# Performance work log

Hardware: AMD Instinct MI355X
Metric: run time of the kernel (lower is better)

The kernel has to match this reference:

```python
import jax, jax.numpy as jnp
import numpy as np

B, S, HID, NH, D = 8, 1024, 768, 12, 64
LENGTHS = np.array([1024, 896, 768, 640, 1024, 512, 768, 896], dtype=np.int64)


def setup_inputs() -> dict:
    key = jax.random.key(0)
    k1, k2 = jax.random.split(key)
    total = int(LENGTHS.sum())  # 6528

    cu_seqlens = jnp.asarray(np.concatenate([[0], np.cumsum(LENGTHS)]), dtype=jnp.int32)
    # flattened (b*s) positions of valid tokens, per flash-attn bert_padding
    indices = jnp.asarray(
        np.concatenate([b * S + np.arange(L) for b, L in enumerate(LENGTHS)]),
        dtype=jnp.int64)
    # 0 = valid token, 1 = pad (original checks attn_mask == 0 for valid)
    attn_mask = jnp.asarray(
        (np.arange(S)[None, :] >= LENGTHS[:, None]).astype(np.int32))

    hidden_states = jax.random.normal(k1, (total, HID), dtype=jnp.float32) * 0.02
    Wqkv_w = jax.random.normal(k2, (3 * HID, HID), dtype=jnp.float32) * 0.02
    Wqkv_b = jnp.zeros((3 * HID,), dtype=jnp.float32)

    # ALiBi bias fused with padding mask, as mosaic passes alibi_attn_mask
    slopes = 2.0 ** (-8.0 * np.arange(1, NH + 1) / NH)  # (NH,)
    pos = np.arange(S)
    rel = -np.abs(pos[None, :] - pos[:, None]).astype(np.float32)  # (S,S)
    alibi_hss = slopes[:, None, None].astype(np.float32) * rel      # (NH,S,S)
    pad_bias = np.where(np.asarray(attn_mask)[:, None, None, :] == 0, 0.0, -10000.0)
    alibi = jnp.asarray(alibi_hss[None] + pad_bias, dtype=jnp.float32)  # (B,NH,S,S)

    return {
        "hidden_states": hidden_states,
        "Wqkv_w": Wqkv_w,
        "Wqkv_b": Wqkv_b,
        "alibi": alibi,
        "cu_seqlens": cu_seqlens,
        "max_seqlen_in_batch": S,
        "indices": indices,
        "attn_mask": attn_mask,
    }


def reference(hidden_states, Wqkv_w, Wqkv_b, alibi, cu_seqlens,
              max_seqlen_in_batch, indices, attn_mask):
    batch = cu_seqlens.shape[0] - 1
    s = max_seqlen_in_batch
    nh = alibi.shape[1]
    d = hidden_states.shape[1] // nh

    # packed QKV projection on unpadded tokens: (nnz, 3*hid)
    qkv = hidden_states @ Wqkv_w.T + Wqkv_b
    # pad_input: scatter into (b*s, 3*hid), then view (b, s, 3, h, d)
    qkv_pad = jnp.zeros((batch * s, qkv.shape[-1]), dtype=qkv.dtype).at[indices].set(qkv)
    qkv_pad = qkv_pad.reshape(batch, s, 3, nh, d)
    q, k, v = qkv_pad[:, :, 0], qkv_pad[:, :, 1], qkv_pad[:, :, 2]  # (b, s, h, d)

    scale = 1.0 / jnp.sqrt(jnp.asarray(d, dtype=q.dtype))
    scores = jnp.einsum('bshd,bthd->bhst', q, k) * scale + alibi  # (b, h, s, s)
    probs = jax.nn.softmax(scores, axis=-1)
    ctx = jnp.einsum('bhst,bthd->bshd', probs, v)  # (b, s, h, d)

    # unpad_input: gather valid tokens back to (nnz, h*d)
    ctx = ctx.reshape(batch * s, nh * d)[indices]
    return ctx
```

## Files before the change

kernel.cpp:

```cpp
#include <hip/hip_runtime.h>
#include <hip/hip_bf16.h>
#include <stdint.h>


typedef __attribute__((ext_vector_type(8))) __bf16 bf16x8;
typedef __attribute__((ext_vector_type(8))) short short8;
typedef __attribute__((ext_vector_type(4))) short short4v;
typedef __attribute__((ext_vector_type(4))) float f32x4;
typedef __attribute__((ext_vector_type(2))) unsigned int u32x2;
typedef unsigned int u32;

#define AS1 __attribute__((address_space(1)))
#define AS3 __attribute__((address_space(3)))

static __device__ __forceinline__ unsigned short f2bf(float x) {
  unsigned u = __builtin_bit_cast(unsigned, x);
  u += 0x7fffu + ((u >> 16) & 1u);
  return (unsigned short)(u >> 16);
}
static __device__ __forceinline__ bf16x8 ld8s(const short* p) {
  return __builtin_bit_cast(bf16x8, *(const short8*)p);
}
static __device__ __forceinline__ u32 cvtpk(float lo, float hi) {
  u32 r;
  asm("v_cvt_pk_bf16_f32 %0, %1, %2" : "=v"(r) : "v"(lo), "v"(hi));
  return r;
}
static __device__ __forceinline__ f32x4 mfma16(u32x2 a, u32x2 b, f32x4 c) {
  asm("v_mfma_f32_16x16x16_bf16 %0, %1, %2, %0" : "+v"(c) : "v"(a), "v"(b));
  return c;
}
static __device__ __forceinline__ float vexp2(float x) {
  float r;
  asm("v_exp_f32 %0, %1" : "=v"(r) : "v"(x));
  return r;
}

__device__ const float g_slope[12] = {
  0.6299605249f, 0.3968502630f, 0.25f,          0.1574901312f,
  0.0992125657f, 0.0625f,       0.0393725328f,  0.0248031414f,
  0.015625f,     0.0098431332f, 0.0062007854f,  0.00390625f
};

__global__ __launch_bounds__(256) void convert_in(
    const float* __restrict__ hidden, const float* __restrict__ W,
    short* __restrict__ hb, short* __restrict__ wb)
{
  constexpr int NA = 6528 * 768;
  constexpr int NW = 2304 * 768;
  const int tot4 = (NA + NW) / 4;
  for (int idx = blockIdx.x * 256 + threadIdx.x; idx < tot4; idx += gridDim.x * 256) {
    const int e0 = idx * 4;
    const float* src; short* dst; int off;
    if (e0 < NA) { src = hidden; dst = hb; off = e0; }
    else         { src = W;      dst = wb; off = e0 - NA; }
    f32x4 v = *((const f32x4*)(src + off));
    short4v o;
    o[0] = (short)f2bf(v[0]); o[1] = (short)f2bf(v[1]);
    o[2] = (short)f2bf(v[2]); o[3] = (short)f2bf(v[3]);
    *(short4v*)(dst + off) = o;
  }
}

__global__ __launch_bounds__(256, 2) void qkv_gemm(
    const short* __restrict__ A, const short* __restrict__ W,
    const float* __restrict__ bias,
    short* __restrict__ qws, short* __restrict__ kws, short* __restrict__ vtws)
{
  constexpr int CUb[9] = {0,1024,1920,2688,3328,4352,4864,5632,6528};
  __shared__ __align__(16) short As[256 * 64];
  __shared__ __align__(16) short Bs[128 * 64];
  const int tid  = threadIdx.x;
  const int lane = tid & 63, w = tid >> 6;
  const int g = lane >> 4, c = lane & 15;
  const int wm = w >> 1, wn = w & 1;
  const int bm = blockIdx.x, bn = blockIdx.y;

  const short* Ab = A + (size_t)bm * 256 * 768;
  const short* Wb = W + (size_t)bn * 128 * 768;

  f32x4 acc[8][4] = {};
  const int sR8 = lane >> 3;
  const int sC8 = (lane & 7) ^ sR8;

  for (int kt = 0; kt < 12; ++kt) {
    if (kt) __syncthreads();
#pragma unroll
    for (int i = 0; i < 8; ++i) {
      const int j = w * 8 + i;
      const AS1 unsigned int* ga =
        (const AS1 unsigned int*)(Ab + (size_t)(j * 8 + sR8) * 768 + kt * 64 + sC8 * 8);
      __builtin_amdgcn_global_load_lds(ga, (AS3 unsigned int*)&As[j * 512], 16, 0, 0);
    }
#pragma unroll
    for (int i = 0; i < 4; ++i) {
      const int j = w * 4 + i;
      const AS1 unsigned int* gb =
        (const AS1 unsigned int*)(Wb + (size_t)(j * 8 + sR8) * 768 + kt * 64 + sC8 * 8);
      __builtin_amdgcn_global_load_lds(gb, (AS3 unsigned int*)&Bs[j * 512], 16, 0, 0);
    }
    __syncthreads();

#pragma unroll
    for (int kh = 0; kh < 2; ++kh) {
      const int xg = (((kh * 4 + g) ^ (c & 7)) << 3);
      bf16x8 bfr[4];
#pragma unroll
      for (int nt = 0; nt < 4; ++nt)
        bfr[nt] = ld8s(&Bs[(wn * 64 + nt * 16 + c) * 64 + xg]);
#pragma unroll
      for (int mt = 0; mt < 8; ++mt) {
        bf16x8 af = ld8s(&As[(wm * 128 + mt * 16 + c) * 64 + xg]);
#pragma unroll
        for (int nt = 0; nt < 4; ++nt)
          acc[mt][nt] = __builtin_amdgcn_mfma_f32_16x16x32_bf16(af, bfr[nt], acc[mt][nt], 0, 0, 0);
      }
    }
  }

  const int row0 = bm * 256 + wm * 128;
  if (row0 >= 6528) return;
  int b = 0;
#pragma unroll
  for (int i = 0; i < 8; ++i) if (row0 >= CUb[i + 1]) b = i + 1;
  const int col0  = bn * 128 + wn * 64;
  const int which = col0 / 768;
  const int hh    = (col0 % 768) / 64;
  const int srow0 = row0 - CUb[b];

  float bb[4];
#pragma unroll
  for (int nt = 0; nt < 4; ++nt) bb[nt] = bias[col0 + nt * 16 + c];

  if (which < 2) {
    const float sc = which ? 1.0f : 0.18033688011112042f;
    short* dst = (which ? kws : qws) + (size_t)(b * 12 + hh) * 1024 * 64;
#pragma unroll
    for (int mt = 0; mt < 8; ++mt)
#pragma unroll
      for (int nt = 0; nt < 4; ++nt)
#pragma unroll
        for (int r = 0; r < 4; ++r) {
          const int s = srow0 + mt * 16 + g * 4 + r;
          dst[(size_t)s * 64 + nt * 16 + c] = (short)f2bf((acc[mt][nt][r] + bb[nt]) * sc);
        }
  } else {
    short* dst = vtws + (size_t)(b * 12 + hh) * 64 * 1024;
#pragma unroll
    for (int mt = 0; mt < 8; ++mt)
#pragma unroll
      for (int nt = 0; nt < 4; ++nt) {
        const int s = srow0 + mt * 16 + g * 4;
        short4v pk;
        pk[0] = (short)f2bf(acc[mt][nt][0] + bb[nt]);
        pk[1] = (short)f2bf(acc[mt][nt][1] + bb[nt]);
        pk[2] = (short)f2bf(acc[mt][nt][2] + bb[nt]);
        pk[3] = (short)f2bf(acc[mt][nt][3] + bb[nt]);
        *(short4v*)&dst[(size_t)(nt * 16 + c) * 1024 + s] = pk;
      }
  }
}

__global__ __launch_bounds__(256, 2) void attn(
    const short* __restrict__ qws, const short* __restrict__ kws,
    const short* __restrict__ vtws, float* __restrict__ out)
{
  constexpr int CU[9]  = {0,1024,1920,2688,3328,4352,4864,5632,6528};
  constexpr int CQT[9] = {0,8,15,21,26,34,38,44,51};
  __shared__ __align__(16) short Ks[2][64 * 64];
  __shared__ __align__(16) short Vs[2][64 * 64];
  const int tid = threadIdx.x, lane = tid & 63, w = tid >> 6;
  const int g = lane >> 4, c = lane & 15;
  const int h = blockIdx.y;
  const int gq = blockIdx.x;
  int b = 0;
#pragma unroll
  for (int i = 0; i < 8; ++i) if (gq >= CQT[i + 1]) b = i + 1;
  const int qt = gq - CQT[b];
  const int Lb = CU[b + 1] - CU[b];
  const int sb = qt * 128 + w * 32;
  const size_t bh = (size_t)(b * 12 + h) * 1024 * 64;
  const short* qp = qws + bh;
  const short* kp = kws + bh;
  const short* vp = vtws + bh;
  const float slope2 = g_slope[h] * 1.4426950408889634f;

  const int sRow = lane >> 3;
  const int sChk = (lane & 7) ^ (sRow & 7);

  bf16x8 qf[2][2];
#pragma unroll
  for (int qh = 0; qh < 2; ++qh)
#pragma unroll
    for (int ks = 0; ks < 2; ++ks)
      qf[qh][ks] = ld8s(qp + (size_t)(sb + qh * 16 + c) * 64 + ks * 32 + g * 8);

  float srowf[2];
#pragma unroll
  for (int qh = 0; qh < 2; ++qh) srowf[qh] = (float)(sb + qh * 16 + c);

  f32x4 accO[2][4] = {};
  float l_part[2] = {};

  auto kaddr = [&](int row, int chunk) { return row * 64 + ((chunk ^ (row & 7)) << 3); };
  auto vaddr = [&](int row, int nt) {
    return row * 64 + (((2 * nt + (g >> 1)) ^ (row & 7)) << 3) + ((g & 1) << 2);
  };

#pragma unroll
  for (int i = 0; i < 2; ++i) {
    const int j = w * 2 + i;
    const int row = j * 8 + sRow;
    const AS1 unsigned int* gk =
      (const AS1 unsigned int*)(kp + (size_t)row * 64 + sChk * 8);
    __builtin_amdgcn_global_load_lds(gk, (AS3 unsigned int*)&Ks[0][j * 512], 16, 0, 0);
    const AS1 unsigned int* gv =
      (const AS1 unsigned int*)(vp + (size_t)row * 1024 + sChk * 8);
    __builtin_amdgcn_global_load_lds(gv, (AS3 unsigned int*)&Vs[0][j * 512], 16, 0, 0);
  }
  __syncthreads();

  int cur = 0;
  for (int t0 = 0; t0 < Lb; t0 += 64) {
    if (t0 + 64 < Lb) {
#pragma unroll
      for (int i = 0; i < 2; ++i) {
        const int j = w * 2 + i;
        const int row = j * 8 + sRow;
        const AS1 unsigned int* gk =
          (const AS1 unsigned int*)(kp + (size_t)(t0 + 64 + row) * 64 + sChk * 8);
        __builtin_amdgcn_global_load_lds(gk, (AS3 unsigned int*)&Ks[cur ^ 1][j * 512], 16, 0, 0);
        const AS1 unsigned int* gv =
          (const AS1 unsigned int*)(vp + (size_t)row * 1024 + (t0 + 64) + sChk * 8);
        __builtin_amdgcn_global_load_lds(gv, (AS3 unsigned int*)&Vs[cur ^ 1][j * 512], 16, 0, 0);
      }
    }

    f32x4 sa[2][4];
    __builtin_amdgcn_s_setprio(1);
#pragma unroll
    for (int nt = 0; nt < 4; ++nt) {
      bf16x8 kf0 = ld8s(&Ks[cur][kaddr(nt * 16 + c, g)]);
      bf16x8 kf1 = ld8s(&Ks[cur][kaddr(nt * 16 + c, 4 + g)]);
#pragma unroll
      for (int qh = 0; qh < 2; ++qh) {
        f32x4 z = {};
        z = __builtin_amdgcn_mfma_f32_16x16x32_bf16(kf0, qf[qh][0], z, 0, 0, 0);
        sa[qh][nt] = __builtin_amdgcn_mfma_f32_16x16x32_bf16(kf1, qf[qh][1], z, 0, 0, 0);
      }
    }
    __builtin_amdgcn_s_setprio(0);

    u32x2 pa[2][4];
    const float tg = (float)(t0 + g * 4);
#pragma unroll
    for (int qh = 0; qh < 2; ++qh) {
#pragma unroll
      for (int nt = 0; nt < 4; ++nt) {
        float p[4];
#pragma unroll
        for (int r = 0; r < 4; ++r) {
          const float d = srowf[qh] - (tg + (float)(nt * 16 + r));
          p[r] = vexp2(fmaf(-slope2, fabsf(d), sa[qh][nt][r]));
          l_part[qh] += p[r];
        }
        pa[qh][nt][0] = cvtpk(p[0], p[1]);
        pa[qh][nt][1] = cvtpk(p[2], p[3]);
      }
    }

    __builtin_amdgcn_s_setprio(1);
#pragma unroll
    for (int ntd = 0; ntd < 4; ++ntd) {
#pragma unroll
      for (int nt = 0; nt < 4; ++nt) {
        u32x2 vb = *(const u32x2*)&Vs[cur][vaddr(c + 16 * ntd, nt)];
        accO[0][ntd] = mfma16(pa[0][nt], vb, accO[0][ntd]);
        accO[1][ntd] = mfma16(pa[1][nt], vb, accO[1][ntd]);
      }
    }
    __builtin_amdgcn_s_setprio(0);

    __syncthreads();
    cur ^= 1;
  }

  float linv[2][4];
#pragma unroll
  for (int qh = 0; qh < 2; ++qh) {
    float rs = l_part[qh];
    rs += __shfl_xor(rs, 16, 64);
    rs += __shfl_xor(rs, 32, 64);
    const float inv = 1.0f / rs;
#pragma unroll
    for (int r = 0; r < 4; ++r)
      linv[qh][r] = __shfl(inv, g * 4 + r, 64);
  }

#pragma unroll
  for (int qh = 0; qh < 2; ++qh)
#pragma unroll
    for (int r = 0; r < 4; ++r) {
      const int srow = sb + qh * 16 + g * 4 + r;
      const size_t ob = (size_t)(CU[b] + srow) * 768 + h * 64;
#pragma unroll
      for (int ntd = 0; ntd < 4; ++ntd)
        out[ob + ntd * 16 + c] = accO[qh][ntd][r] * linv[qh][r];
    }
}

extern "C" void kernel_launch(void* const* d_in, const int* in_sizes, int n_in,
                              void* d_out, int out_size, void* d_ws, size_t ws_size,
                              hipStream_t stream) {
  const float* hidden = (const float*)d_in[0];
  const float* Wqkv_w = (const float*)d_in[1];
  const float* Wqkv_b = (const float*)d_in[2];

  constexpr size_t NA_PAD = (size_t)6656 * 768;
  constexpr size_t NW = (size_t)2304 * 768;
  constexpr size_t NP = (size_t)8 * 12 * 1024 * 64;

  short* hb   = (short*)d_ws;
  short* wb   = hb + NA_PAD;
  short* qws  = wb + NW;
  short* kws  = qws + NP;
  short* vtws = kws + NP;

  convert_in<<<dim3(2048), 256, 0, stream>>>(hidden, Wqkv_w, hb, wb);
  qkv_gemm<<<dim3(26, 18), 256, 0, stream>>>(hb, wb, Wqkv_b, qws, kws, vtws);
  attn<<<dim3(51, 12), 256, 0, stream>>>(qws, kws, vtws, (float*)d_out);
}
```

Measured before the change: 80.10 us.

## Use 16x16x32 MFMA for PV by permuting K rows at staging

Replaces the sixteen 16x16x16 bf16 MFMAs per output tile in the P·V product with eight 16x16x32 MFMAs. The K tile rows are loaded in permuted order so that the score-accumulator layout lines up with the wider A-operand layout, and the ALiBi distance is computed from the permuted key positions. V fragments are now read as 8-element chunks through the same swizzle used for K. This halves the PV MFMA instruction count and the number of LDS reads, at the cost of a more intricate index mapping that must stay consistent with the row permutation.

```diff
diff --git a/kernel.cpp b/kernel.cpp
--- a/kernel.cpp
+++ b/kernel.cpp
@@ -7,7 +7,7 @@
 typedef __attribute__((ext_vector_type(8))) short short8;
 typedef __attribute__((ext_vector_type(4))) short short4v;
 typedef __attribute__((ext_vector_type(4))) float f32x4;
-typedef __attribute__((ext_vector_type(2))) unsigned int u32x2;
+typedef __attribute__((ext_vector_type(4))) unsigned int u32x4;
 typedef unsigned int u32;
 
 #define AS1 __attribute__((address_space(1)))
@@ -25,10 +25,6 @@
   u32 r;
   asm("v_cvt_pk_bf16_f32 %0, %1, %2" : "=v"(r) : "v"(lo), "v"(hi));
   return r;
-}
-static __device__ __forceinline__ f32x4 mfma16(u32x2 a, u32x2 b, f32x4 c) {
-  asm("v_mfma_f32_16x16x16_bf16 %0, %1, %2, %0" : "+v"(c) : "v"(a), "v"(b));
-  return c;
 }
 static __device__ __forceinline__ float vexp2(float x) {
   float r;
@@ -203,38 +199,30 @@
   float l_part[2] = {};
 
   auto kaddr = [&](int row, int chunk) { return row * 64 + ((chunk ^ (row & 7)) << 3); };
-  auto vaddr = [&](int row, int nt) {
-    return row * 64 + (((2 * nt + (g >> 1)) ^ (row & 7)) << 3) + ((g & 1) << 2);
+  auto fperm = [&](int p) {
+    return (p & 32) | (((p >> 2) & 3) << 3) | (((p >> 4) & 1) << 2) | (p & 3);
   };
 
-#pragma unroll
-  for (int i = 0; i < 2; ++i) {
-    const int j = w * 2 + i;
-    const int row = j * 8 + sRow;
-    const AS1 unsigned int* gk =
-      (const AS1 unsigned int*)(kp + (size_t)row * 64 + sChk * 8);
-    __builtin_amdgcn_global_load_lds(gk, (AS3 unsigned int*)&Ks[0][j * 512], 16, 0, 0);
-    const AS1 unsigned int* gv =
-      (const AS1 unsigned int*)(vp + (size_t)row * 1024 + sChk * 8);
-    __builtin_amdgcn_global_load_lds(gv, (AS3 unsigned int*)&Vs[0][j * 512], 16, 0, 0);
-  }
+  auto stageKV = [&](int t, int buf) {
+#pragma unroll
+    for (int i = 0; i < 2; ++i) {
+      const int j = w * 2 + i;
+      const int dRow = j * 8 + sRow;
+      const AS1 unsigned int* gk =
+        (const AS1 unsigned int*)(kp + (size_t)(t + fperm(dRow)) * 64 + sChk * 8);
+      __builtin_amdgcn_global_load_lds(gk, (AS3 unsigned int*)&Ks[buf][j * 512], 16, 0, 0);
+      const AS1 unsigned int* gv =
+        (const AS1 unsigned int*)(vp + (size_t)dRow * 1024 + t + sChk * 8);
+      __builtin_amdgcn_global_load_lds(gv, (AS3 unsigned int*)&Vs[buf][j * 512], 16, 0, 0);
+    }
+  };
+
+  stageKV(0, 0);
   __syncthreads();
 
   int cur = 0;
   for (int t0 = 0; t0 < Lb; t0 += 64) {
-    if (t0 + 64 < Lb) {
-#pragma unroll
-      for (int i = 0; i < 2; ++i) {
-        const int j = w * 2 + i;
-        const int row = j * 8 + sRow;
-        const AS1 unsigned int* gk =
-          (const AS1 unsigned int*)(kp + (size_t)(t0 + 64 + row) * 64 + sChk * 8);
-        __builtin_amdgcn_global_load_lds(gk, (AS3 unsigned int*)&Ks[cur ^ 1][j * 512], 16, 0, 0);
-        const AS1 unsigned int* gv =
-          (const AS1 unsigned int*)(vp + (size_t)row * 1024 + (t0 + 64) + sChk * 8);
-        __builtin_amdgcn_global_load_lds(gv, (AS3 unsigned int*)&Vs[cur ^ 1][j * 512], 16, 0, 0);
-      }
-    }
+    if (t0 + 64 < Lb) stageKV(t0 + 64, cur ^ 1);
 
     f32x4 sa[2][4];
     __builtin_amdgcn_s_setprio(1);
@@ -251,21 +239,21 @@
     }
     __builtin_amdgcn_s_setprio(0);
 
-    u32x2 pa[2][4];
-    const float tg = (float)(t0 + g * 4);
+    u32x4 pa32[2][2];
 #pragma unroll
     for (int qh = 0; qh < 2; ++qh) {
 #pragma unroll
       for (int nt = 0; nt < 4; ++nt) {
+        const float tg = (float)(t0 + 32 * (nt >> 1) + 4 * (nt & 1) + 8 * g);
         float p[4];
 #pragma unroll
         for (int r = 0; r < 4; ++r) {
-          const float d = srowf[qh] - (tg + (float)(nt * 16 + r));
+          const float d = srowf[qh] - (tg + (float)r);
           p[r] = vexp2(fmaf(-slope2, fabsf(d), sa[qh][nt][r]));
           l_part[qh] += p[r];
         }
-        pa[qh][nt][0] = cvtpk(p[0], p[1]);
-        pa[qh][nt][1] = cvtpk(p[2], p[3]);
+        pa32[qh][nt >> 1][(nt & 1) * 2 + 0] = cvtpk(p[0], p[1]);
+        pa32[qh][nt >> 1][(nt & 1) * 2 + 1] = cvtpk(p[2], p[3]);
       }
     }
 
@@ -273,10 +261,12 @@
 #pragma unroll
     for (int ntd = 0; ntd < 4; ++ntd) {
 #pragma unroll
-      for (int nt = 0; nt < 4; ++nt) {
-        u32x2 vb = *(const u32x2*)&Vs[cur][vaddr(c + 16 * ntd, nt)];
-        accO[0][ntd] = mfma16(pa[0][nt], vb, accO[0][ntd]);
-        accO[1][ntd] = mfma16(pa[1][nt], vb, accO[1][ntd]);
+      for (int s = 0; s < 2; ++s) {
+        bf16x8 vb = ld8s(&Vs[cur][kaddr(c + 16 * ntd, 4 * s + g)]);
+        accO[0][ntd] = __builtin_amdgcn_mfma_f32_16x16x32_bf16(
+            __builtin_bit_cast(bf16x8, pa32[0][s]), vb, accO[0][ntd], 0, 0, 0);
+        accO[1][ntd] = __builtin_amdgcn_mfma_f32_16x16x32_bf16(
+            __builtin_bit_cast(bf16x8, pa32[1][s]), vb, accO[1][ntd], 0, 0, 0);
       }
     }
     __builtin_amdgcn_s_setprio(0);
```

Measured after the change: 77.23 us, median of 2. -3.6%, faster.
